# Performance work log

Measured on AMD Instinct MI355X. Metric: run time of the kernel, lower is better.

The kernel has to match this reference:

```python
import jax, jax.numpy as jnp
import numpy as np

D = 256      # input_dim
H = 8        # n_heads
HD = D // H  # head_dim = 32
S = 255      # num variables
S1 = S + 1   # new_seq (CLS + vars)
B = 4


def setup_inputs() -> dict:
    key = jax.random.key(0)
    ks = jax.random.split(key, 16)
    g = lambda k, shp, s=0.05: (jax.random.normal(k, shp, dtype=jnp.float32) * s)
    inp = {
        'desc_embeddings': jax.random.normal(ks[0], (B, S, D), dtype=jnp.float32),
        'name_value_embeddings': jax.random.normal(ks[1], (B, S1, D), dtype=jnp.float32),
        # q/k/v projections (nn.Linear: y = x @ W.T + b)
        'qW': g(ks[2], (D, D)), 'qb': jnp.zeros((D,), jnp.float32),
        'kW': g(ks[3], (D, D)), 'kb': jnp.zeros((D,), jnp.float32),
        'vW': g(ks[4], (D, D)), 'vb': jnp.zeros((D,), jnp.float32),
        # edge_update MLP: Linear(2D->D), LayerNorm(D), ReLU, Linear(D->D)
        'eW1': g(ks[5], (D, 2 * D)), 'eb1': jnp.zeros((D,), jnp.float32),
        'ln_g': jnp.ones((D,), jnp.float32), 'ln_b': jnp.zeros((D,), jnp.float32),
        'eW2': g(ks[6], (D, D)), 'eb2': jnp.zeros((D,), jnp.float32),
        # attn_proj: Linear(3*head_dim -> 1)
        'aW': g(ks[7], (1, 3 * HD)), 'ab': jnp.zeros((1,), jnp.float32),
    }
    return inp


def reference(desc_embeddings, name_value_embeddings, qW, qb, kW, kb, vW, vb,
              eW1, eb1, ln_g, ln_b, eW2, eb2, aW, ab):
    nve, desc = name_value_embeddings, desc_embeddings
    b, s1, _ = nve.shape
    s = s1 - 1

    # structure mask: CLS->Var on, Var->CLS off, Var-Var fully connected (self loops kept)
    new_adj = jnp.zeros((b, s1, s1), jnp.float32)
    new_adj = new_adj.at[:, 1:, 1:].set(1.0)
    new_adj = new_adj.at[:, 0, 1:].set(1.0)

    def lin(x, W, bb):
        return x @ W.T + bb

    q = lin(nve, qW, qb).reshape(b, s1, H, HD).transpose(0, 2, 1, 3)  # [B,H,S1,HD]
    k = lin(nve, kW, kb).reshape(b, s1, H, HD).transpose(0, 2, 1, 3)
    v = lin(nve, vW, vb).reshape(b, s1, H, HD).transpose(0, 2, 1, 3)

    # pairwise edge attributes [B,S1,S1,2D]
    di = jnp.broadcast_to(desc[:, :, None, :], (b, s, s, D))
    dj = jnp.broadcast_to(desc[:, None, :, :], (b, s, s, D))
    var_edge = jnp.concatenate([di, dj], axis=-1)              # [B,S,S,2D]
    cls_edge = jnp.concatenate([desc, desc], axis=-1)          # [B,S,2D]
    ea = jnp.zeros((b, s1, s1, 2 * D), jnp.float32)
    ea = ea.at[:, 1:, 1:].set(var_edge)
    ea = ea.at[:, 0, 1:].set(cls_edge)
    ea = ea.at[:, 1:, 0].set(cls_edge)

    # edge_update MLP (edge_type == 'mlp')
    h = lin(ea, eW1, eb1)
    mu = jnp.mean(h, axis=-1, keepdims=True)
    var = jnp.var(h, axis=-1, keepdims=True)
    h = ln_g * (h - mu) / jnp.sqrt(var + 1e-5) + ln_b
    h = jax.nn.relu(h)
    e = lin(h, eW2, eb2)                                       # [B,S1,S1,D]
    e = e.reshape(b, s1, s1, H, HD).transpose(0, 3, 1, 2, 4)    # [B,H,S1,S1,HD]
    e = e * new_adj[:, None, :, :, None]

    # attn_proj(cat(q_i, k_j, e_ij)) == q_i.wq + k_j.wk + e_ij.we + bias (gat_v1, no nonlinearity)
    wq, wk, we = aW[0, :HD], aW[0, HD:2 * HD], aW[0, 2 * HD:]
    logits = (jnp.einsum('bhid,d->bhi', q, wq)[:, :, :, None]
              + jnp.einsum('bhjd,d->bhj', k, wk)[:, :, None, :]
              + jnp.einsum('bhijd,d->bhij', e, we) + ab[0])    # [B,H,S1,S1]

    logits = logits + (new_adj[:, None] == 0).astype(logits.dtype) * -1e9
    attn = jax.nn.softmax(logits, axis=-1)                      # dropout omitted (eval)
    ctx = jnp.einsum('bhij,bhjd->bhid', attn, v)
    basis_outputs = ctx.transpose(0, 2, 1, 3)                   # [B,S1,H,HD]
    return basis_outputs, attn
```

## Files before the change

### kernel.cpp

```cpp
#include <hip/hip_runtime.h>
#include <math.h>

#define S 255
#define B 4

typedef _Float16 half8 __attribute__((ext_vector_type(8)));
typedef float f32x4 __attribute__((ext_vector_type(4)));

#define WS_APJ   0
#define WS_BPJ   131072
#define WS_VTF   262144
#define WS_AP    393216
#define WS_MFG   654336
#define WS_CONST 656384
#define WS_QLOG  656392
#define WS_KLOG  664584

#define PLS 272

__device__ __forceinline__ half8 cvt8(float4 a, float4 b) {
    half8 h;
    h[0]=(_Float16)a.x; h[1]=(_Float16)a.y; h[2]=(_Float16)a.z; h[3]=(_Float16)a.w;
    h[4]=(_Float16)b.x; h[5]=(_Float16)b.y; h[6]=(_Float16)b.z; h[7]=(_Float16)b.w;
    return h;
}

__global__ __launch_bounds__(256) void k1(
    const float* __restrict__ desc, const float* __restrict__ nve,
    const float* __restrict__ qW, const float* __restrict__ qb,
    const float* __restrict__ kW, const float* __restrict__ kb,
    const float* __restrict__ vW, const float* __restrict__ vb,
    const float* __restrict__ eW1, const float* __restrict__ eb1,
    const float* __restrict__ eW2, const float* __restrict__ eb2,
    const float* __restrict__ aW, float* __restrict__ ws)
{
    const int blk = blockIdx.x;
    const int tid = threadIdx.x;
    __shared__ _Float16 Af[4096];
    __shared__ _Float16 Bf[4096];
    const int wave = tid >> 6, lane = tid & 63;
    const int m16 = lane & 15, quad = lane >> 4;
    const int sr = tid & 63, sko = (tid >> 6) * 16;
    const half8 z8 = {(_Float16)0,(_Float16)0,(_Float16)0,(_Float16)0,
                      (_Float16)0,(_Float16)0,(_Float16)0,(_Float16)0};

    if (blk < 192) {
        const float *X, *W; int M, wst, wof, jobt, sub = blk;
        if (sub < 64)       { X=nve;  W=vW;  M=1024; wst=256; wof=0;   jobt=0; }
        else if (sub < 128) { X=desc; W=eW1; M=1020; wst=512; wof=0;   jobt=1; sub-=64; }
        else                { X=desc; W=eW1; M=1020; wst=512; wof=256; jobt=2; sub-=128; }
        int mBase = (sub>>2)*64, nBase = (sub&3)*64;
        f32x4 acc[2][2] = {};
        for (int k0 = 0; k0 < 256; k0 += 64) {
            half8 xa[2], wb[2];
            int xr = mBase + sr, wr = nBase + sr;
            #pragma unroll
            for (int hh = 0; hh < 2; hh++) {
                int kk = k0 + sko + hh*8;
                if (xr < M) xa[hh] = cvt8(*(const float4*)&X[xr*256 + kk],
                                          *(const float4*)&X[xr*256 + kk + 4]);
                else xa[hh] = z8;
                wb[hh] = cvt8(*(const float4*)&W[wr*wst + wof + kk],
                              *(const float4*)&W[wr*wst + wof + kk + 4]);
            }
            __syncthreads();
            #pragma unroll
            for (int hh = 0; hh < 2; hh++) {
                int krel = sko + hh*8;
                int c = krel >> 5, q2 = (krel >> 3) & 3;
                int ld = (sr & 15) + 16*q2, rt = sr >> 4;
                *(half8*)&Af[((rt*2 + c)*64 + ld)*8] = xa[hh];
                *(half8*)&Bf[((rt*2 + c)*64 + ld)*8] = wb[hh];
            }
            __syncthreads();
            int rt0 = (wave >> 1)*2, ct0 = (wave & 1)*2;
            #pragma unroll
            for (int c = 0; c < 2; c++) {
                half8 A0 = *(const half8*)&Af[(((rt0    )*2 + c)*64 + lane)*8];
                half8 A1 = *(const half8*)&Af[(((rt0 + 1)*2 + c)*64 + lane)*8];
                half8 B0 = *(const half8*)&Bf[(((ct0    )*2 + c)*64 + lane)*8];
                half8 B1 = *(const half8*)&Bf[(((ct0 + 1)*2 + c)*64 + lane)*8];
                acc[0][0] = __builtin_amdgcn_mfma_f32_16x16x32_f16(A0, B0, acc[0][0], 0,0,0);
                acc[0][1] = __builtin_amdgcn_mfma_f32_16x16x32_f16(A0, B1, acc[0][1], 0,0,0);
                acc[1][0] = __builtin_amdgcn_mfma_f32_16x16x32_f16(A1, B0, acc[1][0], 0,0,0);
                acc[1][1] = __builtin_amdgcn_mfma_f32_16x16x32_f16(A1, B1, acc[1][1], 0,0,0);
            }
        }
        int rt0 = (wave >> 1)*2, ct0 = (wave & 1)*2;
        if (jobt == 0) {
            _Float16* vtf = (_Float16*)(ws + WS_VTF);
            #pragma unroll
            for (int ci = 0; ci < 2; ci++) {
                int col = nBase + (ct0 + ci)*16 + m16;
                float bv = vb[col];
                int ct = col >> 4, n = col & 15;
                #pragma unroll
                for (int ri = 0; ri < 2; ri++)
                    #pragma unroll
                    for (int r = 0; r < 4; r++) {
                        int rr = mBase + (rt0 + ri)*16 + quad*4 + r;
                        int bb = rr >> 8, j = rr & 255;
                        int js = j >> 5, qv = (j >> 3) & 3, ev = j & 7;
                        float o = acc[ri][ci][r] + bv;
                        vtf[bb*65536 + (((ct*8 + js)*64 + n + 16*qv) << 3) + ev] = (_Float16)o;
                    }
            }
        } else {
            _Float16* OJ = (_Float16*)(ws + ((jobt == 1) ? WS_APJ : WS_BPJ));
            #pragma unroll
            for (int ci = 0; ci < 2; ci++) {
                int col = nBase + (ct0 + ci)*16 + m16;
                float bv = (jobt == 1) ? eb1[col] : 0.f;
                int ks = col >> 5, q = (col >> 3) & 3, e = col & 7;
                #pragma unroll
                for (int ri = 0; ri < 2; ri++)
                    #pragma unroll
                    for (int r = 0; r < 4; r++) {
                        int rr = mBase + (rt0 + ri)*16 + quad*4 + r;
                        if (rr < 1020) {
                            float o = acc[ri][ci][r] + bv;
                            int bb = rr / 255;
                            int j = rr - bb*255 + 1;
                            int jt = j >> 4, mm = j & 15;
                            OJ[bb*65536 + (((jt*8 + ks)*64 + mm + 16*q) << 3) + e] = (_Float16)o;
                            if (jobt == 1) ws[WS_AP + rr*256 + col] = o;
                        }
                    }
            }
        }
    } else if (blk < 208) {
        {
            int d = tid;
            float f[16] = {0,0,0,0,0,0,0,0,0,0,0,0,0,0,0,0};
            for (int hd = 0; hd < 32; hd++) {
                float wq = aW[hd], wk = aW[32+hd];
                #pragma unroll
                for (int h = 0; h < 8; h++) {
                    f[h]   = fmaf(wq, qW[(h*32+hd)*256 + d], f[h]);
                    f[8+h] = fmaf(wk, kW[(h*32+hd)*256 + d], f[8+h]);
                }
            }
            int ksd = d >> 5, q2 = (d >> 3) & 3, jj = d & 7;
            #pragma unroll
            for (int n = 0; n < 16; n++)
                Bf[((ksd*64 + n + 16*q2))*8 + jj] = (_Float16)f[n];
        }
        __syncthreads();
        int mBase = (blk - 192)*64;
        f32x4 acc = {0.f,0.f,0.f,0.f};
        for (int k0 = 0; k0 < 256; k0 += 64) {
            half8 xa[2];
            #pragma unroll
            for (int hh = 0; hh < 2; hh++) {
                int kk = k0 + sko + hh*8;
                xa[hh] = cvt8(*(const float4*)&nve[(mBase + sr)*256 + kk],
                              *(const float4*)&nve[(mBase + sr)*256 + kk + 4]);
            }
            __syncthreads();
            #pragma unroll
            for (int hh = 0; hh < 2; hh++) {
                int krel = sko + hh*8;
                int c = krel >> 5, q2 = (krel >> 3) & 3;
                int ld = (sr & 15) + 16*q2, rt = sr >> 4;
                *(half8*)&Af[((rt*2 + c)*64 + ld)*8] = xa[hh];
            }
            __syncthreads();
            #pragma unroll
            for (int c = 0; c < 2; c++) {
                half8 A  = *(const half8*)&Af[((wave*2 + c)*64 + lane)*8];
                half8 Bv = *(const half8*)&Bf[(((k0 >> 5) + c)*64 + lane)*8];
                acc = __builtin_amdgcn_mfma_f32_16x16x32_f16(A, Bv, acc, 0,0,0);
            }
        }
        #pragma unroll
        for (int r = 0; r < 4; r++) {
            int rr = mBase + wave*16 + quad*4 + r;
            int bb = rr >> 8, tt2 = rr & 255;
            if (m16 < 8) ws[WS_QLOG + (bb*8 + m16)*256 + tt2] = acc[r];
            else         ws[WS_KLOG + (bb*8 + m16 - 8)*256 + tt2] = acc[r];
        }
    } else {
        _Float16* mfg = (_Float16*)(ws + WS_MFG);
        int k = tid;
        float a8[8] = {0,0,0,0,0,0,0,0};
        for (int hd = 0; hd < 32; hd++) {
            float we = aW[64+hd];
            #pragma unroll
            for (int h = 0; h < 8; h++)
                a8[h] = fmaf(we, eW2[(h*32+hd)*256 + k], a8[h]);
        }
        int ksd = k >> 5, q2 = (k >> 3) & 3, jj = k & 7;
        #pragma unroll
        for (int h = 0; h < 8; h++)
            mfg[((ksd*64 + h + 16*q2))*8 + jj] = (_Float16)a8[h];
        #pragma unroll
        for (int n = 8; n < 16; n++)
            mfg[((ksd*64 + n + 16*q2))*8 + jj] = (_Float16)0.f;
        {
            _Float16* apj = (_Float16*)(ws + WS_APJ);
            _Float16* bpj = (_Float16*)(ws + WS_BPJ);
            int ks0 = tid >> 5, qz = (tid >> 3) & 3, ez = tid & 7;
            int ad = ((ks0*64 + 16*qz) << 3) + ez;
            #pragma unroll
            for (int bb = 0; bb < 4; bb++) {
                apj[bb*65536 + ad] = (_Float16)0.f;
                bpj[bb*65536 + ad] = (_Float16)0.f;
            }
        }
        {
            int h = tid >> 5, hd = tid & 31;
            float c = aW[64+hd]*eb2[h*32+hd] + aW[hd]*qb[h*32+hd] + aW[32+hd]*kb[h*32+hd];
            #pragma unroll
            for (int off = 16; off >= 1; off >>= 1)
                c += __shfl_xor(c, off, 32);
            if (hd == 0) ws[WS_CONST + h] = c;
        }
    }
}

__global__ __launch_bounds__(512, 4) void k3(
    const float* __restrict__ ln_g, const float* __restrict__ ln_b,
    const float* __restrict__ ab, const float* __restrict__ ws,
    float* __restrict__ out)
{
    const int b = blockIdx.y, gx = blockIdx.x;
    const int i0 = gx*2, i1 = gx*2 + 1;
    const int tid = threadIdx.x;
    const int wave = tid >> 6, lane = tid & 63;
    const int m16 = lane & 15, quad = lane >> 4;
    const bool sp = (gx == 0);

    __shared__ float klds[2048];
    __shared__ float PL0[8*PLS], PL1[8*PLS];
    __shared__ float gL[256], bL[256], aL0[256], aL1[256];
    __shared__ float2 st0[256], st1[256];
    __shared__ float stG0[256], stG1[256], stSB[256], stQB[256], stSA[256], stQA[256];
    __shared__ float baseh[16], sms[16], saqa[16];

    const half8 z8 = {(_Float16)0,(_Float16)0,(_Float16)0,(_Float16)0,
                      (_Float16)0,(_Float16)0,(_Float16)0,(_Float16)0};
    half8 ones8;
    #pragma unroll
    for (int e = 0; e < 8; e++) ones8[e] = (_Float16)1.0f;

    #pragma unroll
    for (int t = 0; t < 4; t++)
        klds[tid + t*512] = ws[WS_KLOG + b*2048 + tid + t*512];
    if (tid < 256) { gL[tid] = ln_g[tid]; bL[tid] = ln_b[tid]; }
    {
        int hf = tid >> 8, t8 = tid & 255;
        int ih = hf ? i1 : i0;
        float av = (ih >= 1) ? ws[WS_AP + ((size_t)(b*S + ih - 1))*256 + t8] : 0.f;
        (hf ? aL1 : aL0)[t8] = av;
        float s1 = av, s2 = av*av;
        #pragma unroll
        for (int off = 32; off >= 1; off >>= 1) {
            s1 += __shfl_xor(s1, off, 64);
            s2 += __shfl_xor(s2, off, 64);
        }
        int hw = wave >> 2, sub = wave & 3;
        if (lane == 0) { saqa[hw*8 + sub] = s1; saqa[hw*8 + 4 + sub] = s2; }
    }
    if (tid < 16) {
        int h = tid & 7, ih = (tid >> 3) ? i1 : i0;
        baseh[tid] = ws[WS_QLOG + (b*8+h)*256 + ih] + ab[0] + ws[WS_CONST + h];
    }
    __syncthreads();

    const _Float16* mfg = (const _Float16*)(ws + WS_MFG);
    const _Float16* bpj = (const _Float16*)(ws + WS_BPJ) + b*65536;
    const _Float16* apj = (const _Float16*)(ws + WS_APJ) + b*65536;
    const _Float16* vtf = (const _Float16*)(ws + WS_VTF) + b*65536;

    if (!sp) {
        #pragma unroll
        for (int t2 = 0; t2 < 2; t2++) {
            int tl = wave*2 + t2;
            f32x4 accGS = {}, accQB = {};
            #pragma unroll
            for (int ks = 0; ks < 8; ks++) {
                half8 bb = *(const half8*)&bpj[((tl*8+ks)*64 + lane) << 3];
                half8 ags;
                if (m16 == 0)
                    ags = cvt8(*(const float4*)&aL0[ks*32 + quad*8],
                               *(const float4*)&aL0[ks*32 + quad*8 + 4]);
                else if (m16 == 1)
                    ags = cvt8(*(const float4*)&aL1[ks*32 + quad*8],
                               *(const float4*)&aL1[ks*32 + quad*8 + 4]);
                else if (m16 == 2) ags = ones8;
                else ags = z8;
                accGS = __builtin_amdgcn_mfma_f32_16x16x32_f16(ags, bb, accGS, 0,0,0);
                accQB = __builtin_amdgcn_mfma_f32_16x16x32_f16(bb,  bb, accQB, 0,0,0);
            }
            int j = tl*16 + m16;
            if (quad == 0) { stG0[j] = accGS[0]; stG1[j] = accGS[1]; stSB[j] = accGS[2]; }
            if (quad == (m16 >> 2)) stQB[j] = accQB[m16 & 3];
        }
    } else {
        #pragma unroll
        for (int t2 = 0; t2 < 2; t2++) {
            int tl = wave*2 + t2;
            f32x4 accSB = {}, accSA = {}, accG = {}, accQA = {}, accQB = {}, accG1 = {};
            #pragma unroll
            for (int ks = 0; ks < 8; ks++) {
                int idx = ((tl*8+ks)*64 + lane) << 3;
                half8 bb = *(const half8*)&bpj[idx];
                half8 aa = *(const half8*)&apj[idx];
                half8 a1 = (m16 == 0) ? ones8 : z8;
                half8 ag1;
                if (m16 == 0)
                    ag1 = cvt8(*(const float4*)&aL1[ks*32 + quad*8],
                               *(const float4*)&aL1[ks*32 + quad*8 + 4]);
                else ag1 = z8;
                accSB = __builtin_amdgcn_mfma_f32_16x16x32_f16(a1, bb, accSB, 0,0,0);
                accSA = __builtin_amdgcn_mfma_f32_16x16x32_f16(a1, aa, accSA, 0,0,0);
                accG  = __builtin_amdgcn_mfma_f32_16x16x32_f16(aa, bb, accG,  0,0,0);
                accQA = __builtin_amdgcn_mfma_f32_16x16x32_f16(aa, aa, accQA, 0,0,0);
                accQB = __builtin_amdgcn_mfma_f32_16x16x32_f16(bb, bb, accQB, 0,0,0);
                accG1 = __builtin_amdgcn_mfma_f32_16x16x32_f16(ag1, bb, accG1, 0,0,0);
            }
            int j = tl*16 + m16;
            if (quad == 0) { stSB[j] = accSB[0]; stSA[j] = accSA[0]; stG1[j] = accG1[0]; }
            if (quad == (m16 >> 2)) {
                int r = m16 & 3;
                stG0[j] = accG[r]; stQA[j] = accQA[r]; stQB[j] = accQB[r];
            }
        }
    }
    __syncthreads();

    {
        int hf = tid >> 8, j = tid & 255;
        float2 v; v.x = 0.f; v.y = 0.f;
        if (j >= 1) {
            float sa, qa;
            if (sp && hf == 0) { sa = stSA[j]; qa = stQA[j]; }
            else {
                int base = hf ? 8 : 0;
                sa = saqa[base+0] + saqa[base+1] + saqa[base+2] + saqa[base+3];
                qa = saqa[base+4] + saqa[base+5] + saqa[base+6] + saqa[base+7];
            }
            float g = hf ? stG1[j] : stG0[j];
            float sb = stSB[j], qb2 = stQB[j];
            float mu  = (sa + sb) * (1.0f/256.0f);
            float var = (qa + qb2 + 2.f*g) * (1.0f/256.0f) - mu*mu;
            float inv = rsqrtf(var + 1e-5f);
            v.x = inv; v.y = -mu*inv;
        }
        (hf ? st1 : st0)[j] = v;
    }
    __syncthreads();

    f32x4 acc[2][2] = {};
    float2 sv0[2], sv1[2];
    #pragma unroll
    for (int tt = 0; tt < 2; tt++) {
        sv0[tt] = st0[(wave*2 + tt)*16 + m16];
        sv1[tt] = st1[(wave*2 + tt)*16 + m16];
    }

    #pragma unroll
    for (int ks = 0; ks < 8; ks++) {
        int k = ks*32 + quad*8;
        float4 a00 = *(const float4*)&aL0[k], a01 = *(const float4*)&aL0[k+4];
        float4 a10 = *(const float4*)&aL1[k], a11 = *(const float4*)&aL1[k+4];
        float4 g0 = *(const float4*)&gL[k], g1 = *(const float4*)&gL[k+4];
        float4 b0 = *(const float4*)&bL[k], b1 = *(const float4*)&bL[k+4];
        half8 bf = *(const half8*)&mfg[(ks*64 + lane) << 3];
        float aa0[8] = {a00.x,a00.y,a00.z,a00.w,a01.x,a01.y,a01.z,a01.w};
        float aa1[8] = {a10.x,a10.y,a10.z,a10.w,a11.x,a11.y,a11.z,a11.w};
        float ga[8] = {g0.x,g0.y,g0.z,g0.w,g1.x,g1.y,g1.z,g1.w};
        float be[8] = {b0.x,b0.y,b0.z,b0.w,b1.x,b1.y,b1.z,b1.w};
        #pragma unroll
        for (int tt = 0; tt < 2; tt++) {
            int idx2 = ((((wave*2 + tt)*8 + ks)*64 + lane) << 3);
            half8 bp = *(const half8*)&bpj[idx2];
            half8 app = sp ? *(const half8*)&apj[idx2] : z8;
            half8 af0, af1;
            #pragma unroll
            for (int e = 0; e < 8; e++) {
                float bpe = (float)bp[e];
                float c0 = (sp ? (float)app[e] : aa0[e]) + bpe;
                float w0 = fmaf(fmaf(c0, sv0[tt].x, sv0[tt].y), ga[e], be[e]);
                af0[e] = (_Float16)fmaxf(w0, 0.f);
                float c1 = aa1[e] + bpe;
                float w1 = fmaf(fmaf(c1, sv1[tt].x, sv1[tt].y), ga[e], be[e]);
                af1[e] = (_Float16)fmaxf(w1, 0.f);
            }
            acc[0][tt] = __builtin_amdgcn_mfma_f32_16x16x32_f16(af0, bf, acc[0][tt], 0,0,0);
            acc[1][tt] = __builtin_amdgcn_mfma_f32_16x16x32_f16(af1, bf, acc[1][tt], 0,0,0);
        }
    }

    if (m16 < 8) {
        float basev0 = baseh[m16], basev1 = baseh[8 + m16];
        #pragma unroll
        for (int tt = 0; tt < 2; tt++)
            #pragma unroll
            for (int r = 0; r < 4; r++) {
                int jr = (wave*2 + tt)*16 + quad*4 + r;
                float kv = klds[m16*256 + jr];
                float v0 = basev0 + kv + ((jr == 0) ? -1e9f : acc[0][tt][r]);
                float v1 = basev1 + kv + ((jr == 0) ? -1e9f : acc[1][tt][r]);
                PL0[m16*PLS + jr] = v0;
                PL1[m16*PLS + jr] = v1;
            }
    }
    __syncthreads();

    float* attnOut = out + 262144;
    #pragma unroll
    for (int hh = 0; hh < 2; hh++) {
        int row = wave*2 + hh;
        int ihf = row >> 3, h = row & 7;
        float* PLp = ihf ? PL1 : PL0;
        int iv = ihf ? i1 : i0;
        float4 v = *(const float4*)&PLp[h*PLS + lane*4];
        float mv = fmaxf(fmaxf(v.x, v.y), fmaxf(v.z, v.w));
        #pragma unroll
        for (int off = 32; off >= 1; off >>= 1)
            mv = fmaxf(mv, __shfl_xor(mv, off, 64));
        float4 p;
        p.x = __expf(v.x - mv); p.y = __expf(v.y - mv);
        p.z = __expf(v.z - mv); p.w = __expf(v.w - mv);
        float ss = p.x + p.y + p.z + p.w;
        #pragma unroll
        for (int off = 32; off >= 1; off >>= 1)
            ss += __shfl_xor(ss, off, 64);
        *(float4*)&PLp[h*PLS + lane*4] = p;
        if (lane == 0) sms[row] = ss;
        float rs = 1.0f / ss;
        float4 ao;
        ao.x = p.x*rs; ao.y = p.y*rs; ao.z = p.z*rs; ao.w = p.w*rs;
        *(float4*)&attnOut[((b*8+h)*256 + iv)*256 + lane*4] = ao;
    }
    __syncthreads();

    {
        f32x4 cacc[2][2] = {};
        int ct0 = wave*2;
        #pragma unroll
        for (int js = 0; js < 8; js++) {
            half8 af0, af1;
            if (m16 < 8) {
                float4 p00 = *(const float4*)&PL0[m16*PLS + js*32 + quad*8];
                float4 p01 = *(const float4*)&PL0[m16*PLS + js*32 + quad*8 + 4];
                af0 = cvt8(p00, p01);
                float4 p10 = *(const float4*)&PL1[m16*PLS + js*32 + quad*8];
                float4 p11 = *(const float4*)&PL1[m16*PLS + js*32 + quad*8 + 4];
                af1 = cvt8(p10, p11);
            } else { af0 = z8; af1 = z8; }
            #pragma unroll
            for (int cl = 0; cl < 2; cl++) {
                half8 bf = *(const half8*)&vtf[(((ct0+cl)*8 + js)*64 + lane) << 3];
                cacc[0][cl] = __builtin_amdgcn_mfma_f32_16x16x32_f16(af0, bf, cacc[0][cl], 0,0,0);
                cacc[1][cl] = __builtin_amdgcn_mfma_f32_16x16x32_f16(af1, bf, cacc[1][cl], 0,0,0);
            }
        }
        #pragma unroll
        for (int cl = 0; cl < 2; cl++) {
            int ct = ct0 + cl;
            int h = ct >> 1;
            if (quad == (h >> 2)) {
                out[(b*256 + i0)*256 + ct*16 + m16] = cacc[0][cl][h & 3] * (1.0f / sms[h]);
                out[(b*256 + i1)*256 + ct*16 + m16] = cacc[1][cl][h & 3] * (1.0f / sms[8 + h]);
            }
        }
    }
}

extern "C" void kernel_launch(void* const* d_in, const int* in_sizes, int n_in,
                              void* d_out, int out_size, void* d_ws, size_t ws_size,
                              hipStream_t stream)
{
    const float* desc = (const float*)d_in[0];
    const float* nve  = (const float*)d_in[1];
    const float* qW   = (const float*)d_in[2];
    const float* qb   = (const float*)d_in[3];
    const float* kW   = (const float*)d_in[4];
    const float* kb   = (const float*)d_in[5];
    const float* vW   = (const float*)d_in[6];
    const float* vb   = (const float*)d_in[7];
    const float* eW1  = (const float*)d_in[8];
    const float* eb1  = (const float*)d_in[9];
    const float* ln_g = (const float*)d_in[10];
    const float* ln_b = (const float*)d_in[11];
    const float* eW2  = (const float*)d_in[12];
    const float* eb2  = (const float*)d_in[13];
    const float* aW   = (const float*)d_in[14];
    const float* ab   = (const float*)d_in[15];
    float* ws  = (float*)d_ws;
    float* out = (float*)d_out;

    k1<<<dim3(209), 256, 0, stream>>>(desc, nve, qW, qb, kW, kb, vW, vb,
                                      eW1, eb1, eW2, eb2, aW, ws);
    k3<<<dim3(128, 4), 512, 0, stream>>>(ln_g, ln_b, ab, ws, out);
}
```

Measured before the change: 125.9 us.

## Process four query rows per k3 block with 1024 threads

```diff
diff --git a/kernel.cpp b/kernel.cpp
--- a/kernel.cpp
+++ b/kernel.cpp
@@ -16,7 +16,7 @@
 #define WS_QLOG  656392
 #define WS_KLOG  664584
 
-#define PLS 272
+#define PLS 264
 
 __device__ __forceinline__ half8 cvt8(float4 a, float4 b) {
     half8 h;
@@ -218,24 +218,26 @@
     }
 }
 
-__global__ __launch_bounds__(512, 4) void k3(
+__global__ __launch_bounds__(1024, 4) void k3(
     const float* __restrict__ ln_g, const float* __restrict__ ln_b,
     const float* __restrict__ ab, const float* __restrict__ ws,
     float* __restrict__ out)
 {
     const int b = blockIdx.y, gx = blockIdx.x;
-    const int i0 = gx*2, i1 = gx*2 + 1;
+    const int i_base = gx*4;
     const int tid = threadIdx.x;
     const int wave = tid >> 6, lane = tid & 63;
     const int m16 = lane & 15, quad = lane >> 4;
     const bool sp = (gx == 0);
 
     __shared__ float klds[2048];
-    __shared__ float PL0[8*PLS], PL1[8*PLS];
-    __shared__ float gL[256], bL[256], aL0[256], aL1[256];
-    __shared__ float2 st0[256], st1[256];
-    __shared__ float stG0[256], stG1[256], stSB[256], stQB[256], stSA[256], stQA[256];
-    __shared__ float baseh[16], sms[16], saqa[16];
+    __shared__ float PL[4][8*PLS];
+    __shared__ float gL[256], bL[256];
+    __shared__ float aLs[4][256];
+    __shared__ float2 st[4][256];
+    __shared__ float stG[4][256];
+    __shared__ float stSB[256], stQB[256], stSA[256], stQA[256];
+    __shared__ float baseh[32], sms[32], saqa[32];
 
     const half8 z8 = {(_Float16)0,(_Float16)0,(_Float16)0,(_Float16)0,
                       (_Float16)0,(_Float16)0,(_Float16)0,(_Float16)0};
@@ -244,14 +246,15 @@
     for (int e = 0; e < 8; e++) ones8[e] = (_Float16)1.0f;
 
     #pragma unroll
-    for (int t = 0; t < 4; t++)
-        klds[tid + t*512] = ws[WS_KLOG + b*2048 + tid + t*512];
-    if (tid < 256) { gL[tid] = ln_g[tid]; bL[tid] = ln_b[tid]; }
+    for (int t = 0; t < 2; t++)
+        klds[tid + t*1024] = ws[WS_KLOG + b*2048 + tid + t*1024];
+    if (tid < 256) { gL[tid] = ln_g[tid]; }
+    else if (tid < 512) { bL[tid-256] = ln_b[tid-256]; }
     {
         int hf = tid >> 8, t8 = tid & 255;
-        int ih = hf ? i1 : i0;
+        int ih = i_base + hf;
         float av = (ih >= 1) ? ws[WS_AP + ((size_t)(b*S + ih - 1))*256 + t8] : 0.f;
-        (hf ? aL1 : aL0)[t8] = av;
+        aLs[hf][t8] = av;
         float s1 = av, s2 = av*av;
         #pragma unroll
         for (int off = 32; off >= 1; off >>= 1) {
@@ -261,9 +264,9 @@
         int hw = wave >> 2, sub = wave & 3;
         if (lane == 0) { saqa[hw*8 + sub] = s1; saqa[hw*8 + 4 + sub] = s2; }
     }
-    if (tid < 16) {
-        int h = tid & 7, ih = (tid >> 3) ? i1 : i0;
-        baseh[tid] = ws[WS_QLOG + (b*8+h)*256 + ih] + ab[0] + ws[WS_CONST + h];
+    if (tid < 32) {
+        int h = tid & 7, ihf = tid >> 3;
+        baseh[tid] = ws[WS_QLOG + (b*8+h)*256 + (i_base + ihf)] + ab[0] + ws[WS_CONST + h];
     }
     __syncthreads();
 
@@ -273,58 +276,55 @@
     const _Float16* vtf = (const _Float16*)(ws + WS_VTF) + b*65536;
 
     if (!sp) {
-        #pragma unroll
-        for (int t2 = 0; t2 < 2; t2++) {
-            int tl = wave*2 + t2;
-            f32x4 accGS = {}, accQB = {};
-            #pragma unroll
-            for (int ks = 0; ks < 8; ks++) {
-                half8 bb = *(const half8*)&bpj[((tl*8+ks)*64 + lane) << 3];
-                half8 ags;
-                if (m16 == 0)
-                    ags = cvt8(*(const float4*)&aL0[ks*32 + quad*8],
-                               *(const float4*)&aL0[ks*32 + quad*8 + 4]);
-                else if (m16 == 1)
-                    ags = cvt8(*(const float4*)&aL1[ks*32 + quad*8],
-                               *(const float4*)&aL1[ks*32 + quad*8 + 4]);
-                else if (m16 == 2) ags = ones8;
-                else ags = z8;
-                accGS = __builtin_amdgcn_mfma_f32_16x16x32_f16(ags, bb, accGS, 0,0,0);
-                accQB = __builtin_amdgcn_mfma_f32_16x16x32_f16(bb,  bb, accQB, 0,0,0);
-            }
-            int j = tl*16 + m16;
-            if (quad == 0) { stG0[j] = accGS[0]; stG1[j] = accGS[1]; stSB[j] = accGS[2]; }
-            if (quad == (m16 >> 2)) stQB[j] = accQB[m16 & 3];
-        }
+        f32x4 accGS = {}, accQB = {};
+        #pragma unroll
+        for (int ks = 0; ks < 8; ks++) {
+            half8 bb = *(const half8*)&bpj[((wave*8+ks)*64 + lane) << 3];
+            half8 ags;
+            if (m16 < 4)
+                ags = cvt8(*(const float4*)&aLs[m16][ks*32 + quad*8],
+                           *(const float4*)&aLs[m16][ks*32 + quad*8 + 4]);
+            else if (m16 == 4) ags = ones8;
+            else ags = z8;
+            accGS = __builtin_amdgcn_mfma_f32_16x16x32_f16(ags, bb, accGS, 0,0,0);
+            accQB = __builtin_amdgcn_mfma_f32_16x16x32_f16(bb,  bb, accQB, 0,0,0);
+        }
+        int j = wave*16 + m16;
+        if (quad == 0) {
+            stG[0][j] = accGS[0]; stG[1][j] = accGS[1];
+            stG[2][j] = accGS[2]; stG[3][j] = accGS[3];
+        }
+        if (quad == 1) stSB[j] = accGS[0];
+        if (quad == (m16 >> 2)) stQB[j] = accQB[m16 & 3];
     } else {
-        #pragma unroll
-        for (int t2 = 0; t2 < 2; t2++) {
-            int tl = wave*2 + t2;
-            f32x4 accSB = {}, accSA = {}, accG = {}, accQA = {}, accQB = {}, accG1 = {};
-            #pragma unroll
-            for (int ks = 0; ks < 8; ks++) {
-                int idx = ((tl*8+ks)*64 + lane) << 3;
-                half8 bb = *(const half8*)&bpj[idx];
-                half8 aa = *(const half8*)&apj[idx];
-                half8 a1 = (m16 == 0) ? ones8 : z8;
-                half8 ag1;
-                if (m16 == 0)
-                    ag1 = cvt8(*(const float4*)&aL1[ks*32 + quad*8],
-                               *(const float4*)&aL1[ks*32 + quad*8 + 4]);
-                else ag1 = z8;
-                accSB = __builtin_amdgcn_mfma_f32_16x16x32_f16(a1, bb, accSB, 0,0,0);
-                accSA = __builtin_amdgcn_mfma_f32_16x16x32_f16(a1, aa, accSA, 0,0,0);
-                accG  = __builtin_amdgcn_mfma_f32_16x16x32_f16(aa, bb, accG,  0,0,0);
-                accQA = __builtin_amdgcn_mfma_f32_16x16x32_f16(aa, aa, accQA, 0,0,0);
-                accQB = __builtin_amdgcn_mfma_f32_16x16x32_f16(bb, bb, accQB, 0,0,0);
-                accG1 = __builtin_amdgcn_mfma_f32_16x16x32_f16(ag1, bb, accG1, 0,0,0);
-            }
-            int j = tl*16 + m16;
-            if (quad == 0) { stSB[j] = accSB[0]; stSA[j] = accSA[0]; stG1[j] = accG1[0]; }
-            if (quad == (m16 >> 2)) {
-                int r = m16 & 3;
-                stG0[j] = accG[r]; stQA[j] = accQA[r]; stQB[j] = accQB[r];
-            }
+        f32x4 accX = {}, accSA = {}, accG0 = {}, accQA = {}, accQB = {};
+        #pragma unroll
+        for (int ks = 0; ks < 8; ks++) {
+            int idx = ((wave*8+ks)*64 + lane) << 3;
+            half8 bb = *(const half8*)&bpj[idx];
+            half8 aa = *(const half8*)&apj[idx];
+            half8 a1 = (m16 == 0) ? ones8 : z8;
+            half8 agsX;
+            if (m16 < 3)
+                agsX = cvt8(*(const float4*)&aLs[m16+1][ks*32 + quad*8],
+                            *(const float4*)&aLs[m16+1][ks*32 + quad*8 + 4]);
+            else if (m16 == 3) agsX = ones8;
+            else agsX = z8;
+            accX  = __builtin_amdgcn_mfma_f32_16x16x32_f16(agsX, bb, accX,  0,0,0);
+            accSA = __builtin_amdgcn_mfma_f32_16x16x32_f16(a1,   aa, accSA, 0,0,0);
+            accG0 = __builtin_amdgcn_mfma_f32_16x16x32_f16(aa,   bb, accG0, 0,0,0);
+            accQA = __builtin_amdgcn_mfma_f32_16x16x32_f16(aa,   aa, accQA, 0,0,0);
+            accQB = __builtin_amdgcn_mfma_f32_16x16x32_f16(bb,   bb, accQB, 0,0,0);
+        }
+        int j = wave*16 + m16;
+        if (quad == 0) {
+            stG[1][j] = accX[0]; stG[2][j] = accX[1]; stG[3][j] = accX[2];
+            stSB[j] = accX[3];
+            stSA[j] = accSA[0];
+        }
+        if (quad == (m16 >> 2)) {
+            int r = m16 & 3;
+            stG[0][j] = accG0[r]; stQA[j] = accQA[r]; stQB[j] = accQB[r];
         }
     }
     __syncthreads();
@@ -336,75 +336,67 @@
             float sa, qa;
             if (sp && hf == 0) { sa = stSA[j]; qa = stQA[j]; }
             else {
-                int base = hf ? 8 : 0;
+                int base = hf*8;
                 sa = saqa[base+0] + saqa[base+1] + saqa[base+2] + saqa[base+3];
                 qa = saqa[base+4] + saqa[base+5] + saqa[base+6] + saqa[base+7];
             }
-            float g = hf ? stG1[j] : stG0[j];
+            float g = stG[hf][j];
             float sb = stSB[j], qb2 = stQB[j];
             float mu  = (sa + sb) * (1.0f/256.0f);
             float var = (qa + qb2 + 2.f*g) * (1.0f/256.0f) - mu*mu;
             float inv = rsqrtf(var + 1e-5f);
             v.x = inv; v.y = -mu*inv;
         }
-        (hf ? st1 : st0)[j] = v;
+        st[hf][j] = v;
     }
     __syncthreads();
 
-    f32x4 acc[2][2] = {};
-    float2 sv0[2], sv1[2];
+    f32x4 acc[4] = {};
+    float2 sv[4];
     #pragma unroll
-    for (int tt = 0; tt < 2; tt++) {
-        sv0[tt] = st0[(wave*2 + tt)*16 + m16];
-        sv1[tt] = st1[(wave*2 + tt)*16 + m16];
-    }
+    for (int ii = 0; ii < 4; ii++)
+        sv[ii] = st[ii][wave*16 + m16];
 
     #pragma unroll
     for (int ks = 0; ks < 8; ks++) {
         int k = ks*32 + quad*8;
-        float4 a00 = *(const float4*)&aL0[k], a01 = *(const float4*)&aL0[k+4];
-        float4 a10 = *(const float4*)&aL1[k], a11 = *(const float4*)&aL1[k+4];
         float4 g0 = *(const float4*)&gL[k], g1 = *(const float4*)&gL[k+4];
         float4 b0 = *(const float4*)&bL[k], b1 = *(const float4*)&bL[k+4];
         half8 bf = *(const half8*)&mfg[(ks*64 + lane) << 3];
-        float aa0[8] = {a00.x,a00.y,a00.z,a00.w,a01.x,a01.y,a01.z,a01.w};
-        float aa1[8] = {a10.x,a10.y,a10.z,a10.w,a11.x,a11.y,a11.z,a11.w};
+        int idx2 = ((wave*8 + ks)*64 + lane) << 3;
+        half8 bp = *(const half8*)&bpj[idx2];
+        half8 app = sp ? *(const half8*)&apj[idx2] : z8;
         float ga[8] = {g0.x,g0.y,g0.z,g0.w,g1.x,g1.y,g1.z,g1.w};
         float be[8] = {b0.x,b0.y,b0.z,b0.w,b1.x,b1.y,b1.z,b1.w};
         #pragma unroll
-        for (int tt = 0; tt < 2; tt++) {
-            int idx2 = ((((wave*2 + tt)*8 + ks)*64 + lane) << 3);
-            half8 bp = *(const half8*)&bpj[idx2];
-            half8 app = sp ? *(const half8*)&apj[idx2] : z8;
-            half8 af0, af1;
+        for (int ii = 0; ii < 4; ii++) {
+            float4 x0 = *(const float4*)&aLs[ii][k];
+            float4 x1 = *(const float4*)&aLs[ii][k+4];
+            float aa[8] = {x0.x,x0.y,x0.z,x0.w,x1.x,x1.y,x1.z,x1.w};
+            half8 af;
             #pragma unroll
             for (int e = 0; e < 8; e++) {
                 float bpe = (float)bp[e];
-                float c0 = (sp ? (float)app[e] : aa0[e]) + bpe;
-                float w0 = fmaf(fmaf(c0, sv0[tt].x, sv0[tt].y), ga[e], be[e]);
-                af0[e] = (_Float16)fmaxf(w0, 0.f);
-                float c1 = aa1[e] + bpe;
-                float w1 = fmaf(fmaf(c1, sv1[tt].x, sv1[tt].y), ga[e], be[e]);
-                af1[e] = (_Float16)fmaxf(w1, 0.f);
-            }
-            acc[0][tt] = __builtin_amdgcn_mfma_f32_16x16x32_f16(af0, bf, acc[0][tt], 0,0,0);
-            acc[1][tt] = __builtin_amdgcn_mfma_f32_16x16x32_f16(af1, bf, acc[1][tt], 0,0,0);
+                float c = ((sp && ii == 0) ? (float)app[e] : aa[e]) + bpe;
+                float w = fmaf(fmaf(c, sv[ii].x, sv[ii].y), ga[e], be[e]);
+                af[e] = (_Float16)fmaxf(w, 0.f);
+            }
+            acc[ii] = __builtin_amdgcn_mfma_f32_16x16x32_f16(af, bf, acc[ii], 0,0,0);
         }
     }
 
     if (m16 < 8) {
-        float basev0 = baseh[m16], basev1 = baseh[8 + m16];
-        #pragma unroll
-        for (int tt = 0; tt < 2; tt++)
+        #pragma unroll
+        for (int ii = 0; ii < 4; ii++) {
+            float basev = baseh[ii*8 + m16];
             #pragma unroll
             for (int r = 0; r < 4; r++) {
-                int jr = (wave*2 + tt)*16 + quad*4 + r;
-                float kv = klds[m16*256 + jr];
-                float v0 = basev0 + kv + ((jr == 0) ? -1e9f : acc[0][tt][r]);
-                float v1 = basev1 + kv + ((jr == 0) ? -1e9f : acc[1][tt][r]);
-                PL0[m16*PLS + jr] = v0;
-                PL1[m16*PLS + jr] = v1;
-            }
+                int jr = wave*16 + quad*4 + r;
+                float val = basev + klds[m16*256 + jr];
+                val += (jr == 0) ? -1e9f : acc[ii][r];
+                PL[ii][m16*PLS + jr] = val;
+            }
+        }
     }
     __syncthreads();
 
@@ -413,8 +405,8 @@
     for (int hh = 0; hh < 2; hh++) {
         int row = wave*2 + hh;
         int ihf = row >> 3, h = row & 7;
-        float* PLp = ihf ? PL1 : PL0;
-        int iv = ihf ? i1 : i0;
+        float* PLp = PL[ihf];
+        int iv = i_base + ihf;
         float4 v = *(const float4*)&PLp[h*PLS + lane*4];
         float mv = fmaxf(fmaxf(v.x, v.y), fmaxf(v.z, v.w));
         #pragma unroll
@@ -437,33 +429,28 @@
     __syncthreads();
 
     {
-        f32x4 cacc[2][2] = {};
-        int ct0 = wave*2;
+        f32x4 cacc[4] = {};
+        int ct = wave;
         #pragma unroll
         for (int js = 0; js < 8; js++) {
-            half8 af0, af1;
-            if (m16 < 8) {
-                float4 p00 = *(const float4*)&PL0[m16*PLS + js*32 + quad*8];
-                float4 p01 = *(const float4*)&PL0[m16*PLS + js*32 + quad*8 + 4];
-                af0 = cvt8(p00, p01);
-                float4 p10 = *(const float4*)&PL1[m16*PLS + js*32 + quad*8];
-                float4 p11 = *(const float4*)&PL1[m16*PLS + js*32 + quad*8 + 4];
-                af1 = cvt8(p10, p11);
-            } else { af0 = z8; af1 = z8; }
-            #pragma unroll
-            for (int cl = 0; cl < 2; cl++) {
-                half8 bf = *(const half8*)&vtf[(((ct0+cl)*8 + js)*64 + lane) << 3];
-                cacc[0][cl] = __builtin_amdgcn_mfma_f32_16x16x32_f16(af0, bf, cacc[0][cl], 0,0,0);
-                cacc[1][cl] = __builtin_amdgcn_mfma_f32_16x16x32_f16(af1, bf, cacc[1][cl], 0,0,0);
-            }
-        }
-        #pragma unroll
-        for (int cl = 0; cl < 2; cl++) {
-            int ct = ct0 + cl;
-            int h = ct >> 1;
-            if (quad == (h >> 2)) {
-                out[(b*256 + i0)*256 + ct*16 + m16] = cacc[0][cl][h & 3] * (1.0f / sms[h]);
-                out[(b*256 + i1)*256 + ct*16 + m16] = cacc[1][cl][h & 3] * (1.0f / sms[8 + h]);
+            half8 bf = *(const half8*)&vtf[((ct*8 + js)*64 + lane) << 3];
+            #pragma unroll
+            for (int ii = 0; ii < 4; ii++) {
+                half8 af;
+                if (m16 < 8) {
+                    float4 p0 = *(const float4*)&PL[ii][m16*PLS + js*32 + quad*8];
+                    float4 p1 = *(const float4*)&PL[ii][m16*PLS + js*32 + quad*8 + 4];
+                    af = cvt8(p0, p1);
+                } else af = z8;
+                cacc[ii] = __builtin_amdgcn_mfma_f32_16x16x32_f16(af, bf, cacc[ii], 0,0,0);
+            }
+        }
+        int h = ct >> 1;
+        if (quad == (h >> 2)) {
+            #pragma unroll
+            for (int ii = 0; ii < 4; ii++) {
+                out[(b*256 + i_base + ii)*256 + ct*16 + m16]
+                    = cacc[ii][h & 3] * (1.0f / sms[ii*8 + h]);
             }
         }
     }
@@ -494,5 +481,5 @@
 
     k1<<<dim3(209), 256, 0, stream>>>(desc, nve, qW, qb, kW, kb, vW, vb,
                                       eW1, eb1, eW2, eb2, aW, ws);
-    k3<<<dim3(128, 4), 512, 0, stream>>>(ln_g, ln_b, ab, ws, out);
+    k3<<<dim3(64, 4), 1024, 0, stream>>>(ln_g, ln_b, ab, ws, out);
 }
```

Result: slower. 129.8 us (+3.1%).
